# Kernel optimization log

Measured on AMD Instinct MI355X. Metric: run time of the kernel, lower is better.

## Reference

```python
import jax, jax.numpy as jnp
import numpy as np

EPS = 1e-5
NEG = -1e9

def rmsnorm(x, g, eps=EPS):
    x32 = x.astype(jnp.float32)
    n = x32 * jax.lax.rsqrt(jnp.mean(x32 * x32, axis=-1, keepdims=True) + eps)
    return g * n.astype(x.dtype)

def setup_inputs() -> dict:
    key = jax.random.key(0)
    ks = jax.random.split(key, 10)
    B, S, D, H = 2, 2048, 768, 12
    F = 4 * D
    s = 0.02
    return {
        "x": jax.random.normal(ks[0], (B, S, D), jnp.float32),
        "mask": jax.random.randint(ks[1], (B, S, S), 0, 2, jnp.int32),
        "wq": jax.random.normal(ks[2], (D, D), jnp.float32) * s,
        "wk": jax.random.normal(ks[3], (D, D), jnp.float32) * s,
        "wv": jax.random.normal(ks[4], (D, D), jnp.float32) * s,
        "wo": jax.random.normal(ks[5], (D, D), jnp.float32) * s,
        "w1": jax.random.normal(ks[6], (F, D), jnp.float32) * s,
        "w2": jax.random.normal(ks[7], (D, F), jnp.float32) * s,
        "w3": jax.random.normal(ks[8], (F, D), jnp.float32) * s,
        "g_attn": jnp.ones((D,), jnp.float32),
        "g_ffn": jnp.ones((D,), jnp.float32),
    }

def reference(x, mask, wq, wk, wv, wo, w1, w2, w3, g_attn, g_ffn):
    B, S, D = x.shape
    H = 12
    Dk = D // H
    # --- attention sub-block (pre-norm) ---
    xn = rmsnorm(x, g_attn)
    # torch Linear: y = x @ W^T; split heads -> [B,H,S,Dk]
    q = (xn @ wq.T).reshape(B, S, H, Dk).transpose(0, 2, 1, 3)
    k = (xn @ wk.T).reshape(B, S, H, Dk).transpose(0, 2, 1, 3)
    v = (xn @ wv.T).reshape(B, S, H, Dk).transpose(0, 2, 1, 3)
    scores = jnp.einsum("bhqd,bhkd->bhqk", q, k) / jnp.sqrt(jnp.float32(Dk))
    scores = jnp.where(mask[:, None, :, :] == 0, jnp.float32(NEG), scores)
    probs = jax.nn.softmax(scores, axis=-1)  # dropout p=0.0 -> identity
    attn = jnp.einsum("bhqk,bhkd->bhqd", probs, v)
    attn = attn.transpose(0, 2, 1, 3).reshape(B, S, D)
    h = x + attn @ wo.T
    # --- SwiGLU FFN sub-block (pre-norm) ---
    hn = rmsnorm(h, g_ffn)
    ffn = (jax.nn.silu(hn @ w1.T) * (hn @ w3.T)) @ w2.T
    return h + ffn
```

## Files before the change

kernel.cpp:

```cpp
#include <hip/hip_runtime.h>
#include <hip/hip_bf16.h>

#define S_LEN 2048
#define D_MODEL 768
#define NH 12
#define DK 64
#define F_DIM 3072
#define BATCH 2
#define M_ROWS (BATCH * S_LEN)

typedef __bf16 bf16x8 __attribute__((ext_vector_type(8)));
typedef float floatx4 __attribute__((ext_vector_type(4)));
typedef unsigned short u16;
typedef unsigned long long u64;

__device__ inline float bf2f(u16 u) {
    union { unsigned int i; float f; } x; x.i = ((unsigned int)u) << 16; return x.f;
}
__device__ inline u16 f2bf(float f) {
    union { float f; unsigned int i; } x; x.f = f;
    unsigned int r = x.i + 0x7fffu + ((x.i >> 16) & 1u);
    return (u16)(r >> 16);
}
__device__ __forceinline__ bf16x8 as_bf16x8(uint4 v) {
    union { uint4 u; bf16x8 b; } c; c.u = v; return c.b;
}

__device__ __forceinline__ void ldsload16(const u16* g, u16* l) {
    __builtin_amdgcn_global_load_lds(
        (const __attribute__((address_space(1))) unsigned int*)g,
        (__attribute__((address_space(3))) unsigned int*)l, 16, 0, 0);
}

__global__ __launch_bounds__(256)
void cvt_all(const float4* __restrict__ wq, const float4* __restrict__ wk,
             const float4* __restrict__ wv, const float4* __restrict__ wo,
             const float4* __restrict__ w1, const float4* __restrict__ w2,
             const float4* __restrict__ w3,
             ushort4* wqb, ushort4* wkb, ushort4* wvb, ushort4* wob,
             ushort4* w13f, ushort4* w2b) {
    const int WS4 = (D_MODEL * D_MODEL) / 4;
    const int WB4 = (F_DIM * D_MODEL) / 4;
    const int RW4 = D_MODEL / 4;
    int i = blockIdx.x * 256 + threadIdx.x;
    const float4* src; ushort4* dst; int off, doff;
    if (i < 4 * WS4) {
        int s = i / WS4; off = i - s * WS4; doff = off;
        src = (s == 0) ? wq : (s == 1) ? wk : (s == 2) ? wv : wo;
        dst = (s == 0) ? wqb : (s == 1) ? wkb : (s == 2) ? wvb : wob;
    } else {
        int j = i - 4 * WS4; int s = j / WB4; off = j - s * WB4;
        if (s == 1) { src = w2; dst = w2b; doff = off; }
        else {
            src = (s == 0) ? w1 : w3;
            dst = w13f;
            int which = (s == 0) ? 0 : 1;
            int row = off / RW4, c4 = off - row * RW4;
            int k = c4 * 4;
            int n_tile = row >> 4, nl = row & 15;
            int k_tile = k >> 5, quad = (k >> 3) & 3, jj = k & 7;
            int lane = quad * 16 + nl;
            int f = (n_tile * 24 + k_tile) * 2 + which;
            doff = (f * 512 + lane * 8 + jj) >> 2;
        }
    }
    float4 v = src[off];
    ushort4 o;
    o.x = f2bf(v.x); o.y = f2bf(v.y); o.z = f2bf(v.z); o.w = f2bf(v.w);
    dst[doff] = o;
}

__global__ __launch_bounds__(256)
void mask_bits(const int* __restrict__ m, u64* __restrict__ bits) {
    size_t gid = (size_t)blockIdx.x * 256 + threadIdx.x;
    u64 b = __ballot(m[gid] != 0);
    if ((threadIdx.x & 63) == 0) bits[gid >> 6] = b;
}

__global__ __launch_bounds__(256)
void rmsnorm_k(const float* __restrict__ x, const float* __restrict__ g, u16* __restrict__ out) {
    int row = blockIdx.x;
    const float* xr = x + (size_t)row * D_MODEL;
    u16* orow = out + (size_t)row * D_MODEL;
    int t = threadIdx.x;
    float v0 = xr[t];
    float v1 = xr[t + 256];
    float v2 = xr[t + 512];
    float ss = v0 * v0 + v1 * v1 + v2 * v2;
    #pragma unroll
    for (int off = 1; off < 64; off <<= 1) ss += __shfl_xor(ss, off);
    __shared__ float red[4];
    if ((t & 63) == 0) red[t >> 6] = ss;
    __syncthreads();
    float tot = red[0] + red[1] + red[2] + red[3];
    float scale = rsqrtf(tot * (1.0f / (float)D_MODEL) + 1e-5f);
    orow[t]       = f2bf(g[t]       * v0 * scale);
    orow[t + 256] = f2bf(g[t + 256] * v1 * scale);
    orow[t + 512] = f2bf(g[t + 512] * v2 * scale);
}

__global__ __launch_bounds__(256, 3)
void gemm_f1(const u16* __restrict__ A, const u16* __restrict__ W13f,
             u16* __restrict__ Cout) {
    const int K = D_MODEL, N = F_DIM;
    __shared__ u16 As[2][64][32];

    int t = threadIdx.x;
    int w = t >> 6, lane = t & 63;
    int lrow = lane & 15, quad = lane >> 4;

    int lid = blockIdx.y * 24 + blockIdx.x;
    int xcd = lid & 7, s = lid >> 3;
    int nb = xcd * 3 + (s % 3);
    int mb = s / 3;
    int mBase = mb * 64;
    int ntile0 = nb * 8 + w * 2;

    int srow = lane >> 2, scol = (lane & 3) * 8;
    const u16* Ag = A + (size_t)(mBase + w * 16 + srow) * K + scol;
    const uint4* Bf = (const uint4*)W13f;

    auto stageA = [&](int k0, int b) {
        ldsload16(Ag + k0, &As[b][w * 16][0]);
    };

    floatx4 zero = {0.f, 0.f, 0.f, 0.f};
    floatx4 acc[4][2], acc2[4][2];
    #pragma unroll
    for (int r = 0; r < 4; ++r)
        #pragma unroll
        for (int c = 0; c < 2; ++c) { acc[r][c] = zero; acc2[r][c] = zero; }

    stageA(0, 0);
    int cur = 0;
    for (int kt = 0; kt < 24; ++kt) {
        uint4 b1v[2], b3v[2];
        #pragma unroll
        for (int c = 0; c < 2; ++c) {
            int f = ((ntile0 + c) * 24 + kt) * 2;
            b1v[c] = Bf[(size_t)f * 64 + lane];
            b3v[c] = Bf[(size_t)(f + 1) * 64 + lane];
        }
        __syncthreads();
        if (kt + 1 < 24) stageA((kt + 1) * 32, cur ^ 1);

        bf16x8 af[4];
        #pragma unroll
        for (int r = 0; r < 4; ++r) af[r] = *(const bf16x8*)&As[cur][r * 16 + lrow][quad * 8];
        #pragma unroll
        for (int c = 0; c < 2; ++c) {
            bf16x8 b1f = as_bf16x8(b1v[c]);
            bf16x8 b3f = as_bf16x8(b3v[c]);
            #pragma unroll
            for (int r = 0; r < 4; ++r) {
                acc[r][c]  = __builtin_amdgcn_mfma_f32_16x16x32_bf16(af[r], b1f, acc[r][c], 0, 0, 0);
                acc2[r][c] = __builtin_amdgcn_mfma_f32_16x16x32_bf16(af[r], b3f, acc2[r][c], 0, 0, 0);
            }
        }
        cur ^= 1;
    }

    #pragma unroll
    for (int r = 0; r < 4; ++r) {
        #pragma unroll
        for (int c = 0; c < 2; ++c) {
            #pragma unroll
            for (int j = 0; j < 4; ++j) {
                int grow = mBase + r * 16 + quad * 4 + j;
                int gcol = nb * 128 + w * 32 + c * 16 + lrow;
                float a = acc[r][c][j];
                Cout[(size_t)grow * N + gcol] = f2bf((a / (1.0f + __expf(-a))) * acc2[r][c][j]);
            }
        }
    }
}

__global__ __launch_bounds__(256, 3)
void gemm64(const u16* __restrict__ A, const u16* __restrict__ B1,
            const float* __restrict__ R, float* __restrict__ Cout, int N, int K) {
    __shared__ u16 As[2][64][32];
    __shared__ u16 Bs[2][64][32];

    int t = threadIdx.x;
    int w = t >> 6, lane = t & 63;
    int mBase = blockIdx.y * 64, nBase = blockIdx.x * 64;
    int lrow = lane & 15, quad = lane >> 4;
    int wm = (w >> 1) * 32, wn = (w & 1) * 32;

    int srow = lane >> 2, scol = (lane & 3) * 8;
    const u16* Ag = A  + (size_t)(mBase + w * 16 + srow) * K + scol;
    const u16* Bg = B1 + (size_t)(nBase + w * 16 + srow) * K + scol;

    auto stage = [&](int k0, int b) {
        ldsload16(Ag + k0, &As[b][w * 16][0]);
        ldsload16(Bg + k0, &Bs[b][w * 16][0]);
    };

    floatx4 zero = {0.f, 0.f, 0.f, 0.f};
    floatx4 acc[2][2];
    #pragma unroll
    for (int r = 0; r < 2; ++r)
        #pragma unroll
        for (int c = 0; c < 2; ++c) acc[r][c] = zero;

    stage(0, 0);
    int cur = 0;
    for (int k0 = 0; k0 < K; k0 += 32) {
        __syncthreads();
        if (k0 + 32 < K) stage(k0 + 32, cur ^ 1);

        bf16x8 af[2], bf[2];
        #pragma unroll
        for (int r = 0; r < 2; ++r) af[r] = *(const bf16x8*)&As[cur][wm + r * 16 + lrow][quad * 8];
        #pragma unroll
        for (int c = 0; c < 2; ++c) bf[c] = *(const bf16x8*)&Bs[cur][wn + c * 16 + lrow][quad * 8];
        #pragma unroll
        for (int r = 0; r < 2; ++r)
            #pragma unroll
            for (int c = 0; c < 2; ++c)
                acc[r][c] = __builtin_amdgcn_mfma_f32_16x16x32_bf16(af[r], bf[c], acc[r][c], 0, 0, 0);
        cur ^= 1;
    }

    #pragma unroll
    for (int r = 0; r < 2; ++r) {
        #pragma unroll
        for (int c = 0; c < 2; ++c) {
            #pragma unroll
            for (int j = 0; j < 4; ++j) {
                int grow = mBase + wm + r * 16 + quad * 4 + j;
                int gcol = nBase + wn + c * 16 + lrow;
                size_t idx = (size_t)grow * N + gcol;
                Cout[idx] = acc[r][c][j] + R[idx];
            }
        }
    }
}

__global__ __launch_bounds__(256, 4)
void gemm_qkv(const u16* __restrict__ A, const u16* __restrict__ wq,
              const u16* __restrict__ wk, const u16* __restrict__ wv,
              u16* __restrict__ qb, u16* __restrict__ kb, u16* __restrict__ vt) {
    const int K = D_MODEL;
    __shared__ u16 As[2][64][32];
    __shared__ u16 Bs[2][128][32];

    int t = threadIdx.x;
    int w = t >> 6, lane = t & 63;
    int nb = blockIdx.x;
    int which = nb / 6;
    int mBase = blockIdx.y * 64, nBase = (nb % 6) * 128;
    const u16* B1 = (which == 0) ? wq : (which == 1) ? wk : wv;
    int lrow = lane & 15, quad = lane >> 4;
    int wm = (w >> 1) * 32, wn = (w & 1) * 64;

    int srow = lane >> 2, scol = (lane & 3) * 8;
    const u16* Ag = A  + (size_t)(mBase + w * 16 + srow) * K + scol;
    const u16* Bg = B1 + (size_t)(nBase + w * 32 + srow) * K + scol;

    auto stage = [&](int k0, int b) {
        ldsload16(Ag + k0, &As[b][w * 16][0]);
        ldsload16(Bg + k0, &Bs[b][w * 32][0]);
        ldsload16(Bg + (size_t)16 * K + k0, &Bs[b][w * 32 + 16][0]);
    };

    floatx4 zero = {0.f, 0.f, 0.f, 0.f};
    floatx4 acc[2][4];
    #pragma unroll
    for (int r = 0; r < 2; ++r)
        #pragma unroll
        for (int c = 0; c < 4; ++c) acc[r][c] = zero;

    stage(0, 0);
    int cur = 0;
    for (int k0 = 0; k0 < K; k0 += 32) {
        __syncthreads();
        if (k0 + 32 < K) stage(k0 + 32, cur ^ 1);
        bf16x8 af[2];
        #pragma unroll
        for (int r = 0; r < 2; ++r) af[r] = *(const bf16x8*)&As[cur][wm + r * 16 + lrow][quad * 8];
        #pragma unroll
        for (int c = 0; c < 4; ++c) {
            bf16x8 bfr = *(const bf16x8*)&Bs[cur][wn + c * 16 + lrow][quad * 8];
            #pragma unroll
            for (int r = 0; r < 2; ++r)
                acc[r][c] = __builtin_amdgcn_mfma_f32_16x16x32_bf16(af[r], bfr, acc[r][c], 0, 0, 0);
        }
        cur ^= 1;
    }

    u16* dst = (which == 0) ? qb : kb;
    const float qscale = 0.18033688011112042f;
    #pragma unroll
    for (int r = 0; r < 2; ++r) {
        #pragma unroll
        for (int c = 0; c < 4; ++c) {
            #pragma unroll
            for (int j = 0; j < 4; ++j) {
                int grow = mBase + wm + r * 16 + quad * 4 + j;
                int gcol = nBase + wn + c * 16 + lrow;
                float val = acc[r][c][j];
                if (which == 2) {
                    int bb = grow >> 11, s = grow & 2047;
                    int hh = gcol >> 6, d = gcol & 63;
                    vt[((((size_t)bb * NH + hh) * DK + d) << 11) + s] = f2bf(val);
                } else {
                    if (which == 0) val *= qscale;
                    dst[(size_t)grow * D_MODEL + gcol] = f2bf(val);
                }
            }
        }
    }
}

__global__ __launch_bounds__(256)
void attn_mfma(const u16* __restrict__ q, const u16* __restrict__ k,
               const u16* __restrict__ vt, const u64* __restrict__ mbits,
               u16* __restrict__ out) {
    __shared__ u16 Qs0[64][32], Qs1[64][32];
    __shared__ u16 Ks0[2][64][32], Ks1[2][64][32];
    __shared__ u16 Vs0[2][64][32], Vs1[2][64][32];
    __shared__ u16 PT[4][16][72];

    int t = threadIdx.x;
    int lane = t & 63;
    int w = t >> 6;
    int lrow = lane & 15;
    int quad = lane >> 4;

    int st0 = blockIdx.x * 64;
    int bh = blockIdx.y;
    int h = bh % NH;
    int b = bh / NH;

    const u16* qbase = q + ((size_t)b * S_LEN + st0) * D_MODEL + h * DK;
    const u16* kbase = k + (size_t)b * S_LEN * D_MODEL + h * DK;
    const u16* vbase = vt + (size_t)bh * DK * S_LEN;
    const u64* bw = mbits + ((size_t)b * S_LEN + st0 + w * 16 + lrow) * (S_LEN / 64);

    int srow = lane >> 2;
    int scol = (lane & 3) * 8;

    const u16* kg = kbase + (size_t)(w * 16 + srow) * D_MODEL + scol;
    const u16* vg = vbase + (size_t)(w * 16 + srow) * S_LEN + scol;

    auto stageKV = [&](int kt, int bsel) {
        ldsload16(kg + (size_t)kt * D_MODEL, &Ks0[bsel][w * 16][0]);
        ldsload16(kg + (size_t)kt * D_MODEL + 32, &Ks1[bsel][w * 16][0]);
        ldsload16(vg + kt, &Vs0[bsel][w * 16][0]);
        ldsload16(vg + kt + 32, &Vs1[bsel][w * 16][0]);
    };

    const u16* qg = qbase + (size_t)(w * 16 + srow) * D_MODEL + scol;
    ldsload16(qg, &Qs0[w * 16][0]);
    ldsload16(qg + 32, &Qs1[w * 16][0]);
    stageKV(0, 0);
    __syncthreads();
    bf16x8 bq0 = *(const bf16x8*)&Qs0[w * 16 + lrow][quad * 8];
    bf16x8 bq1 = *(const bf16x8*)&Qs1[w * 16 + lrow][quad * 8];

    bf16x8 ones;
    {
        union { u16 u; __bf16 b; } o; o.u = 0x3F80;
        #pragma unroll
        for (int j = 0; j < 8; ++j) ones[j] = o.b;
    }

    floatx4 zero = {0.f, 0.f, 0.f, 0.f};
    floatx4 Ot[4] = {zero, zero, zero, zero};
    floatx4 Osum = zero;

    u64 mw = bw[0];
    int cur = 0;
    for (int kt = 0; kt < S_LEN; kt += 64) {
        if (kt + 64 < S_LEN) stageKV(kt + 64, cur ^ 1);
        u64 mw_next = (kt + 64 < S_LEN) ? bw[(kt >> 6) + 1] : 0ull;
        unsigned mlo = (unsigned)mw, mhi = (unsigned)(mw >> 32);

        floatx4 st[4];
        #pragma unroll
        for (int nt = 0; nt < 4; ++nt) {
            bf16x8 ak0 = *(const bf16x8*)&Ks0[cur][nt * 16 + lrow][quad * 8];
            bf16x8 ak1 = *(const bf16x8*)&Ks1[cur][nt * 16 + lrow][quad * 8];
            st[nt] = __builtin_amdgcn_mfma_f32_16x16x32_bf16(ak0, bq0, zero, 0, 0, 0);
            st[nt] = __builtin_amdgcn_mfma_f32_16x16x32_bf16(ak1, bq1, st[nt], 0, 0, 0);
        }

        #pragma unroll
        for (int nt = 0; nt < 4; ++nt) {
            unsigned half = (nt & 2) ? mhi : mlo;
            unsigned tmp = half >> ((nt & 1) * 16 + quad * 4);
            unsigned eu[4];
            #pragma unroll
            for (int j = 0; j < 4; ++j) {
                float e = __builtin_amdgcn_exp2f(st[nt][j]);
                unsigned msk = (unsigned)((int)(tmp << (31 - j)) >> 31);
                eu[j] = __float_as_uint(e) & msk;
            }
            uint2 p;
            p.x = (eu[0] >> 16) | (eu[1] & 0xffff0000u);
            p.y = (eu[2] >> 16) | (eu[3] & 0xffff0000u);
            *(uint2*)&PT[w][lrow][nt * 16 + quad * 4] = p;
        }

        bf16x8 ap0 = *(const bf16x8*)&PT[w][lrow][quad * 8];
        bf16x8 ap1 = *(const bf16x8*)&PT[w][lrow][32 + quad * 8];
        Osum = __builtin_amdgcn_mfma_f32_16x16x32_bf16(ap0, ones, Osum, 0, 0, 0);
        Osum = __builtin_amdgcn_mfma_f32_16x16x32_bf16(ap1, ones, Osum, 0, 0, 0);
        #pragma unroll
        for (int dt = 0; dt < 4; ++dt) {
            bf16x8 bv0 = *(const bf16x8*)&Vs0[cur][dt * 16 + lrow][quad * 8];
            bf16x8 bv1 = *(const bf16x8*)&Vs1[cur][dt * 16 + lrow][quad * 8];
            Ot[dt] = __builtin_amdgcn_mfma_f32_16x16x32_bf16(ap0, bv0, Ot[dt], 0, 0, 0);
            Ot[dt] = __builtin_amdgcn_mfma_f32_16x16x32_bf16(ap1, bv1, Ot[dt], 0, 0, 0);
        }

        __syncthreads();
        cur ^= 1;
        mw = mw_next;
    }

    float invj[4];
    #pragma unroll
    for (int j = 0; j < 4; ++j) invj[j] = 1.0f / Osum[j];

    u16* obase = out + ((size_t)b * S_LEN + st0 + w * 16) * D_MODEL + h * DK;
    #pragma unroll
    for (int dt = 0; dt < 4; ++dt)
        #pragma unroll
        for (int j = 0; j < 4; ++j)
            obase[(size_t)(quad * 4 + j) * D_MODEL + dt * 16 + lrow] = f2bf(Ot[dt][j] * invj[j]);
}

extern "C" void kernel_launch(void* const* d_in, const int* in_sizes, int n_in,
                              void* d_out, int out_size, void* d_ws, size_t ws_size,
                              hipStream_t stream) {
    const float* x      = (const float*)d_in[0];
    const int*   mask   = (const int*)d_in[1];
    const float* wq     = (const float*)d_in[2];
    const float* wk     = (const float*)d_in[3];
    const float* wv     = (const float*)d_in[4];
    const float* wo     = (const float*)d_in[5];
    const float* w1     = (const float*)d_in[6];
    const float* w2     = (const float*)d_in[7];
    const float* w3     = (const float*)d_in[8];
    const float* g_attn = (const float*)d_in[9];
    const float* g_ffn  = (const float*)d_in[10];
    float* out = (float*)d_out;

    const size_t WSMALL = (size_t)D_MODEL * D_MODEL;
    const size_t WBIG   = (size_t)F_DIM * D_MODEL;
    const size_t MD     = (size_t)M_ROWS * D_MODEL;

    char* ws = (char*)d_ws;
    u16* wqb  = (u16*)ws;            ws += WSMALL * 2;
    u16* wkb  = (u16*)ws;            ws += WSMALL * 2;
    u16* wvb  = (u16*)ws;            ws += WSMALL * 2;
    u16* wob  = (u16*)ws;            ws += WSMALL * 2;
    u16* w13f = (u16*)ws;            ws += WBIG * 2 * 2;
    u16* w2b  = (u16*)ws;            ws += WBIG * 2;
    u16* xn  = (u16*)ws;             ws += MD * 2;
    u16* qb  = (u16*)ws;             ws += MD * 2;
    u16* kb  = (u16*)ws;             ws += MD * 2;
    u16* vb  = (u16*)ws;             ws += MD * 2;
    u16* ao  = (u16*)ws;             ws += MD * 2;
    float* hb = (float*)ws;          ws += MD * 4;
    u64* mb  = (u64*)ws;             ws += (size_t)BATCH * S_LEN * (S_LEN / 64) * 8;
    u16* hn = xn;
    u16* ub = qb;
    (void)ws_size; (void)n_in; (void)in_sizes; (void)out_size;

    dim3 blk(256);

    cvt_all<<<9216, blk, 0, stream>>>((const float4*)wq, (const float4*)wk, (const float4*)wv,
                                      (const float4*)wo, (const float4*)w1, (const float4*)w2,
                                      (const float4*)w3,
                                      (ushort4*)wqb, (ushort4*)wkb, (ushort4*)wvb, (ushort4*)wob,
                                      (ushort4*)w13f, (ushort4*)w2b);
    mask_bits<<<(BATCH * S_LEN * S_LEN) / 256, blk, 0, stream>>>(mask, mb);

    rmsnorm_k<<<M_ROWS, blk, 0, stream>>>(x, g_attn, xn);
    gemm_qkv<<<dim3(18, M_ROWS / 64), blk, 0, stream>>>(xn, wqb, wkb, wvb, qb, kb, vb);
    attn_mfma<<<dim3(S_LEN / 64, BATCH * NH), blk, 0, stream>>>(qb, kb, vb, mb, ao);
    gemm64<<<dim3(D_MODEL / 64, M_ROWS / 64), blk, 0, stream>>>(ao, wob, x, hb, D_MODEL, D_MODEL);
    rmsnorm_k<<<M_ROWS, blk, 0, stream>>>((const float*)hb, g_ffn, hn);
    gemm_f1<<<dim3(24, M_ROWS / 64), blk, 0, stream>>>(hn, w13f, ub);
    gemm64<<<dim3(D_MODEL / 64, M_ROWS / 64), blk, 0, stream>>>(ub, w2b, hb, out, D_MODEL, F_DIM);
}
```

Measured before the change: 352.2 us.

## Load V fragments directly to registers and XOR-swizzle K tiles in LDS

The attention kernel no longer stages V^T tiles through shared memory. Each wave now loads its V MFMA operands straight from global memory into registers at the start of each key tile. K tiles stay staged in LDS but use an XOR-swizzled column layout to reduce bank conflicts on fragment reads. This cuts LDS traffic and footprint, at the cost of every wave redundantly fetching the full V tile from global or L2 with exposed latency and higher register pressure.

```diff
diff --git a/kernel.cpp b/kernel.cpp
--- a/kernel.cpp
+++ b/kernel.cpp
@@ -319,7 +319,6 @@
                u16* __restrict__ out) {
     __shared__ u16 Qs0[64][32], Qs1[64][32];
     __shared__ u16 Ks0[2][64][32], Ks1[2][64][32];
-    __shared__ u16 Vs0[2][64][32], Vs1[2][64][32];
     __shared__ u16 PT[4][16][72];
 
     int t = threadIdx.x;
@@ -340,21 +339,21 @@
 
     int srow = lane >> 2;
     int scol = (lane & 3) * 8;
-
-    const u16* kg = kbase + (size_t)(w * 16 + srow) * D_MODEL + scol;
-    const u16* vg = vbase + (size_t)(w * 16 + srow) * S_LEN + scol;
-
-    auto stageKV = [&](int kt, int bsel) {
+    int scolK = ((lane & 3) ^ ((lane >> 3) & 3)) * 8;
+    int rq = (quad ^ ((lrow >> 1) & 3)) * 8;
+
+    const u16* kg = kbase + (size_t)(w * 16 + srow) * D_MODEL + scolK;
+    const u16* vfg = vbase + (size_t)lrow * S_LEN + quad * 8;
+
+    auto stageK = [&](int kt, int bsel) {
         ldsload16(kg + (size_t)kt * D_MODEL, &Ks0[bsel][w * 16][0]);
         ldsload16(kg + (size_t)kt * D_MODEL + 32, &Ks1[bsel][w * 16][0]);
-        ldsload16(vg + kt, &Vs0[bsel][w * 16][0]);
-        ldsload16(vg + kt + 32, &Vs1[bsel][w * 16][0]);
     };
 
     const u16* qg = qbase + (size_t)(w * 16 + srow) * D_MODEL + scol;
     ldsload16(qg, &Qs0[w * 16][0]);
     ldsload16(qg + 32, &Qs1[w * 16][0]);
-    stageKV(0, 0);
+    stageK(0, 0);
     __syncthreads();
     bf16x8 bq0 = *(const bf16x8*)&Qs0[w * 16 + lrow][quad * 8];
     bf16x8 bq1 = *(const bf16x8*)&Qs1[w * 16 + lrow][quad * 8];
@@ -373,15 +372,22 @@
     u64 mw = bw[0];
     int cur = 0;
     for (int kt = 0; kt < S_LEN; kt += 64) {
-        if (kt + 64 < S_LEN) stageKV(kt + 64, cur ^ 1);
+        if (kt + 64 < S_LEN) stageK(kt + 64, cur ^ 1);
+        uint4 va[8];
+        #pragma unroll
+        for (int dt = 0; dt < 4; ++dt) {
+            const u16* p = vfg + (size_t)dt * 16 * S_LEN + kt;
+            va[dt * 2]     = *(const uint4*)p;
+            va[dt * 2 + 1] = *(const uint4*)(p + 32);
+        }
         u64 mw_next = (kt + 64 < S_LEN) ? bw[(kt >> 6) + 1] : 0ull;
         unsigned mlo = (unsigned)mw, mhi = (unsigned)(mw >> 32);
 
         floatx4 st[4];
         #pragma unroll
         for (int nt = 0; nt < 4; ++nt) {
-            bf16x8 ak0 = *(const bf16x8*)&Ks0[cur][nt * 16 + lrow][quad * 8];
-            bf16x8 ak1 = *(const bf16x8*)&Ks1[cur][nt * 16 + lrow][quad * 8];
+            bf16x8 ak0 = *(const bf16x8*)&Ks0[cur][nt * 16 + lrow][rq];
+            bf16x8 ak1 = *(const bf16x8*)&Ks1[cur][nt * 16 + lrow][rq];
             st[nt] = __builtin_amdgcn_mfma_f32_16x16x32_bf16(ak0, bq0, zero, 0, 0, 0);
             st[nt] = __builtin_amdgcn_mfma_f32_16x16x32_bf16(ak1, bq1, st[nt], 0, 0, 0);
         }
@@ -409,8 +415,8 @@
         Osum = __builtin_amdgcn_mfma_f32_16x16x32_bf16(ap1, ones, Osum, 0, 0, 0);
         #pragma unroll
         for (int dt = 0; dt < 4; ++dt) {
-            bf16x8 bv0 = *(const bf16x8*)&Vs0[cur][dt * 16 + lrow][quad * 8];
-            bf16x8 bv1 = *(const bf16x8*)&Vs1[cur][dt * 16 + lrow][quad * 8];
+            bf16x8 bv0 = as_bf16x8(va[dt * 2]);
+            bf16x8 bv1 = as_bf16x8(va[dt * 2 + 1]);
             Ot[dt] = __builtin_amdgcn_mfma_f32_16x16x32_bf16(ap0, bv0, Ot[dt], 0, 0, 0);
             Ot[dt] = __builtin_amdgcn_mfma_f32_16x16x32_bf16(ap1, bv1, Ot[dt], 0, 0, 0);
         }
```

New measurement: 401.4 us. 1.14x slower.

## Process 128 query rows per attention block with swizzled K/V LDS reads

Applied to the files above, without the earlier changes.

The attention kernel now gives each wave 32 query rows in two 16-row chunks instead of 16. Every K/V tile staged in LDS is therefore reused for twice as many queries, which halves K/V global traffic and block count. Q fragments are loaded straight from global memory into registers instead of going through LDS. An XOR swizzle on the K/V staging columns and read offsets aims to reduce LDS bank conflicts. The costs are more accumulator registers, a larger PT buffer, and only 384 blocks, which may lower occupancy and leave some CUs idle.

```diff
diff --git a/kernel.cpp b/kernel.cpp
--- a/kernel.cpp
+++ b/kernel.cpp
@@ -317,10 +317,9 @@
 void attn_mfma(const u16* __restrict__ q, const u16* __restrict__ k,
                const u16* __restrict__ vt, const u64* __restrict__ mbits,
                u16* __restrict__ out) {
-    __shared__ u16 Qs0[64][32], Qs1[64][32];
     __shared__ u16 Ks0[2][64][32], Ks1[2][64][32];
     __shared__ u16 Vs0[2][64][32], Vs1[2][64][32];
-    __shared__ u16 PT[4][16][72];
+    __shared__ u16 PT[4][32][72];
 
     int t = threadIdx.x;
     int lane = t & 63;
@@ -328,36 +327,39 @@
     int lrow = lane & 15;
     int quad = lane >> 4;
 
-    int st0 = blockIdx.x * 64;
+    int st0 = blockIdx.x * 128;
     int bh = blockIdx.y;
     int h = bh % NH;
     int b = bh / NH;
 
-    const u16* qbase = q + ((size_t)b * S_LEN + st0) * D_MODEL + h * DK;
     const u16* kbase = k + (size_t)b * S_LEN * D_MODEL + h * DK;
     const u16* vbase = vt + (size_t)bh * DK * S_LEN;
-    const u64* bw = mbits + ((size_t)b * S_LEN + st0 + w * 16 + lrow) * (S_LEN / 64);
 
     int srow = lane >> 2;
-    int scol = (lane & 3) * 8;
-
-    const u16* kg = kbase + (size_t)(w * 16 + srow) * D_MODEL + scol;
-    const u16* vg = vbase + (size_t)(w * 16 + srow) * S_LEN + scol;
+    int scolS = ((lane & 3) ^ ((lane >> 3) & 3)) * 8;
+    int rq = (quad ^ ((lrow >> 1) & 3)) * 8;
+
+    const u16* kg = kbase + (size_t)(w * 16 + srow) * D_MODEL + scolS;
+    const u16* vg = vbase + (size_t)(w * 16 + srow) * S_LEN + scolS;
 
     auto stageKV = [&](int kt, int bsel) {
-        ldsload16(kg + (size_t)kt * D_MODEL, &Ks0[bsel][w * 16][0]);
+        ldsload16(kg + (size_t)kt * D_MODEL,      &Ks0[bsel][w * 16][0]);
         ldsload16(kg + (size_t)kt * D_MODEL + 32, &Ks1[bsel][w * 16][0]);
-        ldsload16(vg + kt, &Vs0[bsel][w * 16][0]);
+        ldsload16(vg + kt,      &Vs0[bsel][w * 16][0]);
         ldsload16(vg + kt + 32, &Vs1[bsel][w * 16][0]);
     };
 
-    const u16* qg = qbase + (size_t)(w * 16 + srow) * D_MODEL + scol;
-    ldsload16(qg, &Qs0[w * 16][0]);
-    ldsload16(qg + 32, &Qs1[w * 16][0]);
     stageKV(0, 0);
-    __syncthreads();
-    bf16x8 bq0 = *(const bf16x8*)&Qs0[w * 16 + lrow][quad * 8];
-    bf16x8 bq1 = *(const bf16x8*)&Qs1[w * 16 + lrow][quad * 8];
+
+    bf16x8 bq[2][2];
+    {
+        const u16* qrow = q + ((size_t)b * S_LEN + st0 + w * 32 + lrow) * D_MODEL + h * DK + quad * 8;
+        #pragma unroll
+        for (int qc = 0; qc < 2; ++qc) {
+            bq[qc][0] = *(const bf16x8*)(qrow + (size_t)qc * 16 * D_MODEL);
+            bq[qc][1] = *(const bf16x8*)(qrow + (size_t)qc * 16 * D_MODEL + 32);
+        }
+    }
 
     bf16x8 ones;
     {
@@ -367,69 +369,89 @@
     }
 
     floatx4 zero = {0.f, 0.f, 0.f, 0.f};
-    floatx4 Ot[4] = {zero, zero, zero, zero};
-    floatx4 Osum = zero;
-
-    u64 mw = bw[0];
+    floatx4 Ot[4][2];
+    #pragma unroll
+    for (int dt = 0; dt < 4; ++dt) { Ot[dt][0] = zero; Ot[dt][1] = zero; }
+    floatx4 Osum[2] = {zero, zero};
+
+    const u64* bwl = mbits + ((size_t)b * S_LEN + st0 + w * 32 + lrow) * (S_LEN / 64);
+    u64 mw0 = bwl[0];
+    u64 mw1 = bwl[16 * (S_LEN / 64)];
+    __syncthreads();
+
     int cur = 0;
     for (int kt = 0; kt < S_LEN; kt += 64) {
-        if (kt + 64 < S_LEN) stageKV(kt + 64, cur ^ 1);
-        u64 mw_next = (kt + 64 < S_LEN) ? bw[(kt >> 6) + 1] : 0ull;
-        unsigned mlo = (unsigned)mw, mhi = (unsigned)(mw >> 32);
-
-        floatx4 st[4];
+        u64 mwn0 = 0, mwn1 = 0;
+        if (kt + 64 < S_LEN) {
+            stageKV(kt + 64, cur ^ 1);
+            mwn0 = bwl[(kt >> 6) + 1];
+            mwn1 = bwl[16 * (S_LEN / 64) + (kt >> 6) + 1];
+        }
+
         #pragma unroll
         for (int nt = 0; nt < 4; ++nt) {
-            bf16x8 ak0 = *(const bf16x8*)&Ks0[cur][nt * 16 + lrow][quad * 8];
-            bf16x8 ak1 = *(const bf16x8*)&Ks1[cur][nt * 16 + lrow][quad * 8];
-            st[nt] = __builtin_amdgcn_mfma_f32_16x16x32_bf16(ak0, bq0, zero, 0, 0, 0);
-            st[nt] = __builtin_amdgcn_mfma_f32_16x16x32_bf16(ak1, bq1, st[nt], 0, 0, 0);
-        }
-
-        #pragma unroll
-        for (int nt = 0; nt < 4; ++nt) {
-            unsigned half = (nt & 2) ? mhi : mlo;
-            unsigned tmp = half >> ((nt & 1) * 16 + quad * 4);
-            unsigned eu[4];
-            #pragma unroll
-            for (int j = 0; j < 4; ++j) {
-                float e = __builtin_amdgcn_exp2f(st[nt][j]);
-                unsigned msk = (unsigned)((int)(tmp << (31 - j)) >> 31);
-                eu[j] = __float_as_uint(e) & msk;
+            bf16x8 ak0 = *(const bf16x8*)&Ks0[cur][nt * 16 + lrow][rq];
+            bf16x8 ak1 = *(const bf16x8*)&Ks1[cur][nt * 16 + lrow][rq];
+            #pragma unroll
+            for (int qc = 0; qc < 2; ++qc) {
+                floatx4 stv = __builtin_amdgcn_mfma_f32_16x16x32_bf16(ak0, bq[qc][0], zero, 0, 0, 0);
+                stv = __builtin_amdgcn_mfma_f32_16x16x32_bf16(ak1, bq[qc][1], stv, 0, 0, 0);
+                u64 mwq = qc ? mw1 : mw0;
+                unsigned half = (nt & 2) ? (unsigned)(mwq >> 32) : (unsigned)mwq;
+                unsigned tmp = half >> ((nt & 1) * 16 + quad * 4);
+                unsigned eu[4];
+                #pragma unroll
+                for (int j = 0; j < 4; ++j) {
+                    float e = __builtin_amdgcn_exp2f(stv[j]);
+                    unsigned msk = (unsigned)((int)(tmp << (31 - j)) >> 31);
+                    eu[j] = __float_as_uint(e) & msk;
+                }
+                uint2 p;
+                p.x = (eu[0] >> 16) | (eu[1] & 0xffff0000u);
+                p.y = (eu[2] >> 16) | (eu[3] & 0xffff0000u);
+                *(uint2*)&PT[w][qc * 16 + lrow][nt * 16 + quad * 4] = p;
             }
-            uint2 p;
-            p.x = (eu[0] >> 16) | (eu[1] & 0xffff0000u);
-            p.y = (eu[2] >> 16) | (eu[3] & 0xffff0000u);
-            *(uint2*)&PT[w][lrow][nt * 16 + quad * 4] = p;
-        }
-
-        bf16x8 ap0 = *(const bf16x8*)&PT[w][lrow][quad * 8];
-        bf16x8 ap1 = *(const bf16x8*)&PT[w][lrow][32 + quad * 8];
-        Osum = __builtin_amdgcn_mfma_f32_16x16x32_bf16(ap0, ones, Osum, 0, 0, 0);
-        Osum = __builtin_amdgcn_mfma_f32_16x16x32_bf16(ap1, ones, Osum, 0, 0, 0);
+        }
+
+        bf16x8 ap[2][2];
+        #pragma unroll
+        for (int qc = 0; qc < 2; ++qc) {
+            ap[qc][0] = *(const bf16x8*)&PT[w][qc * 16 + lrow][quad * 8];
+            ap[qc][1] = *(const bf16x8*)&PT[w][qc * 16 + lrow][32 + quad * 8];
+            Osum[qc] = __builtin_amdgcn_mfma_f32_16x16x32_bf16(ap[qc][0], ones, Osum[qc], 0, 0, 0);
+            Osum[qc] = __builtin_amdgcn_mfma_f32_16x16x32_bf16(ap[qc][1], ones, Osum[qc], 0, 0, 0);
+        }
         #pragma unroll
         for (int dt = 0; dt < 4; ++dt) {
-            bf16x8 bv0 = *(const bf16x8*)&Vs0[cur][dt * 16 + lrow][quad * 8];
-            bf16x8 bv1 = *(const bf16x8*)&Vs1[cur][dt * 16 + lrow][quad * 8];
-            Ot[dt] = __builtin_amdgcn_mfma_f32_16x16x32_bf16(ap0, bv0, Ot[dt], 0, 0, 0);
-            Ot[dt] = __builtin_amdgcn_mfma_f32_16x16x32_bf16(ap1, bv1, Ot[dt], 0, 0, 0);
+            bf16x8 bv0 = *(const bf16x8*)&Vs0[cur][dt * 16 + lrow][rq];
+            bf16x8 bv1 = *(const bf16x8*)&Vs1[cur][dt * 16 + lrow][rq];
+            #pragma unroll
+            for (int qc = 0; qc < 2; ++qc) {
+                Ot[dt][qc] = __builtin_amdgcn_mfma_f32_16x16x32_bf16(ap[qc][0], bv0, Ot[dt][qc], 0, 0, 0);
+                Ot[dt][qc] = __builtin_amdgcn_mfma_f32_16x16x32_bf16(ap[qc][1], bv1, Ot[dt][qc], 0, 0, 0);
+            }
         }
 
         __syncthreads();
         cur ^= 1;
-        mw = mw_next;
-    }
-
-    float invj[4];
-    #pragma unroll
-    for (int j = 0; j < 4; ++j) invj[j] = 1.0f / Osum[j];
-
-    u16* obase = out + ((size_t)b * S_LEN + st0 + w * 16) * D_MODEL + h * DK;
+        mw0 = mwn0; mw1 = mwn1;
+    }
+
+    float inv[2][4];
+    #pragma unroll
+    for (int qc = 0; qc < 2; ++qc)
+        #pragma unroll
+        for (int j = 0; j < 4; ++j) inv[qc][j] = 1.0f / Osum[qc][j];
+
+    u16* obase = out + ((size_t)b * S_LEN + st0 + w * 32) * D_MODEL + h * DK;
     #pragma unroll
     for (int dt = 0; dt < 4; ++dt)
         #pragma unroll
-        for (int j = 0; j < 4; ++j)
-            obase[(size_t)(quad * 4 + j) * D_MODEL + dt * 16 + lrow] = f2bf(Ot[dt][j] * invj[j]);
+        for (int qc = 0; qc < 2; ++qc)
+            #pragma unroll
+            for (int j = 0; j < 4; ++j)
+                obase[(size_t)(qc * 16 + quad * 4 + j) * D_MODEL + dt * 16 + lrow] =
+                    f2bf(Ot[dt][qc][j] * inv[qc][j]);
 }
 
 extern "C" void kernel_launch(void* const* d_in, const int* in_sizes, int n_in,
@@ -481,7 +503,7 @@
 
     rmsnorm_k<<<M_ROWS, blk, 0, stream>>>(x, g_attn, xn);
     gemm_qkv<<<dim3(18, M_ROWS / 64), blk, 0, stream>>>(xn, wqb, wkb, wvb, qb, kb, vb);
-    attn_mfma<<<dim3(S_LEN / 64, BATCH * NH), blk, 0, stream>>>(qb, kb, vb, mb, ao);
+    attn_mfma<<<dim3(S_LEN / 128, BATCH * NH), blk, 0, stream>>>(qb, kb, vb, mb, ao);
     gemm64<<<dim3(D_MODEL / 64, M_ROWS / 64), blk, 0, stream>>>(ao, wob, x, hb, D_MODEL, D_MODEL);
     rmsnorm_k<<<M_ROWS, blk, 0, stream>>>((const float*)hb, g_ffn, hn);
     gemm_f1<<<dim3(24, M_ROWS / 64), blk, 0, stream>>>(hn, w13f, ub);
```

New measurement: 360.9 us. 2.5% more time.

## Swizzle LDS layouts in gemm64 and attention, deepen gemm64 K tile, load Q directly

Applied to the files above, without the earlier changes.

gemm64 now stages 64-wide K tiles instead of 32, halving the number of barrier iterations, and XOR-swizzles the LDS column chunks to avoid bank conflicts on the MFMA fragment reads. The attention kernel applies a similar XOR swizzle to its K and V LDS tiles. It also reads its Q fragments straight from global memory into registers, dropping the Q shared-memory staging and one barrier. The changes double gemm64's LDS footprint, which may reduce occupancy at 3 blocks per CU, and rely on global loads that are not coalesced for Q.

```diff
diff --git a/kernel.cpp b/kernel.cpp
--- a/kernel.cpp
+++ b/kernel.cpp
@@ -178,8 +178,8 @@
 __global__ __launch_bounds__(256, 3)
 void gemm64(const u16* __restrict__ A, const u16* __restrict__ B1,
             const float* __restrict__ R, float* __restrict__ Cout, int N, int K) {
-    __shared__ u16 As[2][64][32];
-    __shared__ u16 Bs[2][64][32];
+    __shared__ u16 As[2][64][64];
+    __shared__ u16 Bs[2][64][64];
 
     int t = threadIdx.x;
     int w = t >> 6, lane = t & 63;
@@ -187,13 +187,16 @@
     int lrow = lane & 15, quad = lane >> 4;
     int wm = (w >> 1) * 32, wn = (w & 1) * 32;
 
-    int srow = lane >> 2, scol = (lane & 3) * 8;
-    const u16* Ag = A  + (size_t)(mBase + w * 16 + srow) * K + scol;
-    const u16* Bg = B1 + (size_t)(nBase + w * 16 + srow) * K + scol;
+    int srow8 = lane >> 3;
+    int sc64 = ((lane & 7) ^ srow8) * 8;
+    const u16* Ag = A  + (size_t)(mBase + w * 16 + srow8) * K + sc64;
+    const u16* Bg = B1 + (size_t)(nBase + w * 16 + srow8) * K + sc64;
 
     auto stage = [&](int k0, int b) {
-        ldsload16(Ag + k0, &As[b][w * 16][0]);
-        ldsload16(Bg + k0, &Bs[b][w * 16][0]);
+        ldsload16(Ag + k0,                 &As[b][w * 16][0]);
+        ldsload16(Ag + (size_t)8 * K + k0, &As[b][w * 16 + 8][0]);
+        ldsload16(Bg + k0,                 &Bs[b][w * 16][0]);
+        ldsload16(Bg + (size_t)8 * K + k0, &Bs[b][w * 16 + 8][0]);
     };
 
     floatx4 zero = {0.f, 0.f, 0.f, 0.f};
@@ -205,20 +208,24 @@
 
     stage(0, 0);
     int cur = 0;
-    for (int k0 = 0; k0 < K; k0 += 32) {
+    for (int k0 = 0; k0 < K; k0 += 64) {
         __syncthreads();
-        if (k0 + 32 < K) stage(k0 + 32, cur ^ 1);
-
-        bf16x8 af[2], bf[2];
-        #pragma unroll
-        for (int r = 0; r < 2; ++r) af[r] = *(const bf16x8*)&As[cur][wm + r * 16 + lrow][quad * 8];
-        #pragma unroll
-        for (int c = 0; c < 2; ++c) bf[c] = *(const bf16x8*)&Bs[cur][wn + c * 16 + lrow][quad * 8];
-        #pragma unroll
-        for (int r = 0; r < 2; ++r)
-            #pragma unroll
-            for (int c = 0; c < 2; ++c)
-                acc[r][c] = __builtin_amdgcn_mfma_f32_16x16x32_bf16(af[r], bf[c], acc[r][c], 0, 0, 0);
+        if (k0 + 64 < K) stage(k0 + 64, cur ^ 1);
+
+        #pragma unroll
+        for (int half = 0; half < 2; ++half) {
+            int rc = ((half * 4 + quad) ^ (lrow & 7)) * 8;
+            bf16x8 af[2], bf[2];
+            #pragma unroll
+            for (int r = 0; r < 2; ++r) af[r] = *(const bf16x8*)&As[cur][wm + r * 16 + lrow][rc];
+            #pragma unroll
+            for (int c = 0; c < 2; ++c) bf[c] = *(const bf16x8*)&Bs[cur][wn + c * 16 + lrow][rc];
+            #pragma unroll
+            for (int r = 0; r < 2; ++r)
+                #pragma unroll
+                for (int c = 0; c < 2; ++c)
+                    acc[r][c] = __builtin_amdgcn_mfma_f32_16x16x32_bf16(af[r], bf[c], acc[r][c], 0, 0, 0);
+        }
         cur ^= 1;
     }
 
@@ -317,7 +324,6 @@
 void attn_mfma(const u16* __restrict__ q, const u16* __restrict__ k,
                const u16* __restrict__ vt, const u64* __restrict__ mbits,
                u16* __restrict__ out) {
-    __shared__ u16 Qs0[64][32], Qs1[64][32];
     __shared__ u16 Ks0[2][64][32], Ks1[2][64][32];
     __shared__ u16 Vs0[2][64][32], Vs1[2][64][32];
     __shared__ u16 PT[4][16][72];
@@ -333,31 +339,32 @@
     int h = bh % NH;
     int b = bh / NH;
 
-    const u16* qbase = q + ((size_t)b * S_LEN + st0) * D_MODEL + h * DK;
     const u16* kbase = k + (size_t)b * S_LEN * D_MODEL + h * DK;
     const u16* vbase = vt + (size_t)bh * DK * S_LEN;
     const u64* bw = mbits + ((size_t)b * S_LEN + st0 + w * 16 + lrow) * (S_LEN / 64);
 
     int srow = lane >> 2;
-    int scol = (lane & 3) * 8;
-
-    const u16* kg = kbase + (size_t)(w * 16 + srow) * D_MODEL + scol;
-    const u16* vg = vbase + (size_t)(w * 16 + srow) * S_LEN + scol;
+    int scolS = ((lane & 3) ^ ((lane >> 3) & 3)) * 8;
+    int rq = (quad ^ ((lrow >> 1) & 3)) * 8;
+
+    const u16* kg = kbase + (size_t)(w * 16 + srow) * D_MODEL + scolS;
+    const u16* vg = vbase + (size_t)(w * 16 + srow) * S_LEN + scolS;
 
     auto stageKV = [&](int kt, int bsel) {
-        ldsload16(kg + (size_t)kt * D_MODEL, &Ks0[bsel][w * 16][0]);
+        ldsload16(kg + (size_t)kt * D_MODEL,      &Ks0[bsel][w * 16][0]);
         ldsload16(kg + (size_t)kt * D_MODEL + 32, &Ks1[bsel][w * 16][0]);
-        ldsload16(vg + kt, &Vs0[bsel][w * 16][0]);
+        ldsload16(vg + kt,      &Vs0[bsel][w * 16][0]);
         ldsload16(vg + kt + 32, &Vs1[bsel][w * 16][0]);
     };
 
-    const u16* qg = qbase + (size_t)(w * 16 + srow) * D_MODEL + scol;
-    ldsload16(qg, &Qs0[w * 16][0]);
-    ldsload16(qg + 32, &Qs1[w * 16][0]);
     stageKV(0, 0);
-    __syncthreads();
-    bf16x8 bq0 = *(const bf16x8*)&Qs0[w * 16 + lrow][quad * 8];
-    bf16x8 bq1 = *(const bf16x8*)&Qs1[w * 16 + lrow][quad * 8];
+
+    bf16x8 bq0, bq1;
+    {
+        const u16* qrow = q + ((size_t)b * S_LEN + st0 + w * 16 + lrow) * D_MODEL + h * DK + quad * 8;
+        bq0 = *(const bf16x8*)qrow;
+        bq1 = *(const bf16x8*)(qrow + 32);
+    }
 
     bf16x8 ones;
     {
@@ -371,6 +378,8 @@
     floatx4 Osum = zero;
 
     u64 mw = bw[0];
+    __syncthreads();
+
     int cur = 0;
     for (int kt = 0; kt < S_LEN; kt += 64) {
         if (kt + 64 < S_LEN) stageKV(kt + 64, cur ^ 1);
@@ -380,8 +389,8 @@
         floatx4 st[4];
         #pragma unroll
         for (int nt = 0; nt < 4; ++nt) {
-            bf16x8 ak0 = *(const bf16x8*)&Ks0[cur][nt * 16 + lrow][quad * 8];
-            bf16x8 ak1 = *(const bf16x8*)&Ks1[cur][nt * 16 + lrow][quad * 8];
+            bf16x8 ak0 = *(const bf16x8*)&Ks0[cur][nt * 16 + lrow][rq];
+            bf16x8 ak1 = *(const bf16x8*)&Ks1[cur][nt * 16 + lrow][rq];
             st[nt] = __builtin_amdgcn_mfma_f32_16x16x32_bf16(ak0, bq0, zero, 0, 0, 0);
             st[nt] = __builtin_amdgcn_mfma_f32_16x16x32_bf16(ak1, bq1, st[nt], 0, 0, 0);
         }
@@ -409,8 +418,8 @@
         Osum = __builtin_amdgcn_mfma_f32_16x16x32_bf16(ap1, ones, Osum, 0, 0, 0);
         #pragma unroll
         for (int dt = 0; dt < 4; ++dt) {
-            bf16x8 bv0 = *(const bf16x8*)&Vs0[cur][dt * 16 + lrow][quad * 8];
-            bf16x8 bv1 = *(const bf16x8*)&Vs1[cur][dt * 16 + lrow][quad * 8];
+            bf16x8 bv0 = *(const bf16x8*)&Vs0[cur][dt * 16 + lrow][rq];
+            bf16x8 bv1 = *(const bf16x8*)&Vs1[cur][dt * 16 + lrow][rq];
             Ot[dt] = __builtin_amdgcn_mfma_f32_16x16x32_bf16(ap0, bv0, Ot[dt], 0, 0, 0);
             Ot[dt] = __builtin_amdgcn_mfma_f32_16x16x32_bf16(ap1, bv1, Ot[dt], 0, 0, 0);
         }
```

New measurement: 334.8 us. 4.9% less time.
